# Kernel optimization log

Measured on AMD Instinct MI355X. Metric: run time of the kernel, lower is better.

Reference implementation:

```python
import jax, jax.numpy as jnp
import numpy as np

B, N, C, H, D, K = 8, 2000, 64, 64, 16, 2  # batch, nodes, hidden, hidden_hidden, embed_dim, cheb_k


def setup_inputs() -> dict:
    key = jax.random.key(0)
    ks = jax.random.split(key, 12)
    f = lambda k, s, sc=1.0: jax.random.normal(k, s, dtype=jnp.float32) * sc
    return {
        "z": f(ks[0], (B, N, C)),
        "W_in": f(ks[1], (H, C), 0.1),
        "b_in": f(ks[2], (H,), 0.1),
        "W_out": f(ks[3], (C * C, H), 0.05),
        "b_out": f(ks[4], (C * C,), 0.05),
        "emb": f(ks[5], (N, D), 0.1),
        "wp": f(ks[6], (D, K, H, H), 0.1),
        "bp": f(ks[7], (D, H), 0.1),
        "w1": f(ks[8], (C,)),
        "w2": f(ks[9], (C,)),
        "vs": f(ks[10], (N, N), 0.02),
        "bs": f(ks[11], (N, N), 0.02),
    }


def reference(z, W_in, b_in, W_out, b_out, emb, wp, bp, w1, w2, vs, bs):
    # linear_in + relu: (B,N,C) -> (B,N,H)
    h = jax.nn.relu(jnp.einsum("bnc,hc->bnh", z, W_in) + b_in)

    # data-adaptive graph: softmax over rows of relu(emb @ emb^T)
    A = jax.nn.softmax(jax.nn.relu(emb @ emb.T), axis=1)  # (N,N)
    S = jnp.stack([jnp.eye(N, dtype=z.dtype), A], axis=0)  # (K,N,N), cheb_k=2

    # spatial attention on h (x = h.unsqueeze(1), f_in == H == C)
    e1 = h @ w1  # (B,N)
    e2 = h @ w2  # (B,N)
    prod = e1[:, :, None] * e2[:, None, :]  # (B,N,N) outer product
    E = jax.nn.softmax(
        jnp.einsum("nm,bmp->bnp", vs, jax.nn.sigmoid(prod + bs)), axis=-1
    )  # (B,N,N)

    # batched supports: E.unsqueeze(1) @ S -> (B,K,N,N)
    sup = jnp.einsum("bnm,kmp->bknp", E, S)

    # node-adaptive weights / bias
    weights = jnp.einsum("nd,dkio->nkio", emb, wp)  # (N,K,H,H)
    bias = emb @ bp  # (N,H)

    # graph conv
    x_g = jnp.einsum("bknm,bmc->bnkc", sup, h)  # (B,N,K,H)
    g = jnp.einsum("bnki,nkio->bno", x_g, weights) + bias  # (B,N,H)

    # linear_out + view + tanh, scaled by 0.1
    out = jnp.tanh(jnp.einsum("bnh,oh->bno", g, W_out) + b_out)
    return 0.1 * out.reshape(B, N, C, C)
```

## Files before the change

kernel.cpp:

```cpp
#include <hip/hip_runtime.h>
#include <hip/hip_bf16.h>

#define NN 2000
#define NP 2048
#define BB 8
#define HH 64
#define DD 16

typedef __hip_bfloat16 bf16;
typedef short bf16x8 __attribute__((ext_vector_type(8)));
typedef float f32x4 __attribute__((ext_vector_type(4)));

__device__ __forceinline__ float fast_sigmoid(float x) {
    return 1.0f / (1.0f + __expf(-x));
}
__device__ __forceinline__ float fast_tanh(float x) {
    float e = __expf(2.0f * x);
    return 1.0f - 2.0f / (e + 1.0f);
}

__device__ __forceinline__ void glds16(const void* g, void* l) {
    __builtin_amdgcn_global_load_lds(
        (const __attribute__((address_space(1))) void*)g,
        (__attribute__((address_space(3))) void*)l, 16, 0, 0);
}

__global__ __launch_bounds__(256) void k_h(
        const float* __restrict__ z, const float* __restrict__ W_in,
        const float* __restrict__ b_in, const float* __restrict__ w1,
        const float* __restrict__ w2, float* __restrict__ h,
        float* __restrict__ e1, float* __restrict__ e2) {
    __shared__ float WT[64 * 65];
    __shared__ float zs[4][64];
    int t = threadIdx.x;
    int lane = t & 63, ty = t >> 6;
    int bn0 = blockIdx.x * 4;
    for (int i = t; i < 64 * 64; i += 256) {
        int hh = i >> 6, c = i & 63;
        WT[c * 65 + hh] = W_in[i];
    }
    zs[ty][lane] = z[(size_t)(bn0 + ty) * 64 + lane];
    __syncthreads();
    float acc = b_in[lane];
    #pragma unroll
    for (int c = 0; c < 64; c++) acc += zs[ty][c] * WT[c * 65 + lane];
    float hv = fmaxf(acc, 0.0f);
    h[(size_t)(bn0 + ty) * 64 + lane] = hv;
    float p1 = hv * w1[lane], p2 = hv * w2[lane];
    #pragma unroll
    for (int off = 32; off > 0; off >>= 1) {
        p1 += __shfl_down(p1, off);
        p2 += __shfl_down(p2, off);
    }
    if (lane == 0) { e1[bn0 + ty] = p1; e2[bn0 + ty] = p2; }
}

__global__ __launch_bounds__(256) void k_A(const float* __restrict__ emb,
                                           bf16* __restrict__ A) {
    int i = blockIdx.x, t = threadIdx.x;
    if (i >= NN) {
        for (int j = t; j < NP; j += 256) A[(size_t)i * NP + j] = __float2bfloat16(0.0f);
        return;
    }
    __shared__ float ei[DD];
    __shared__ float rowbuf[NP];
    __shared__ float red[256];
    if (t < DD) ei[t] = emb[i * DD + t];
    __syncthreads();
    float lmax = -1e30f;
    for (int j = t; j < NP; j += 256) {
        float s = 0.0f;
        if (j < NN) {
            #pragma unroll
            for (int d = 0; d < DD; d++) s += ei[d] * emb[j * DD + d];
            s = fmaxf(s, 0.0f);
            lmax = fmaxf(lmax, s);
        }
        rowbuf[j] = s;
    }
    red[t] = lmax; __syncthreads();
    for (int o = 128; o > 0; o >>= 1) { if (t < o) red[t] = fmaxf(red[t], red[t + o]); __syncthreads(); }
    float mx = red[0];
    __syncthreads();
    float lsum = 0.0f;
    for (int j = t; j < NN; j += 256) {
        float e = __expf(rowbuf[j] - mx);
        rowbuf[j] = e; lsum += e;
    }
    red[t] = lsum; __syncthreads();
    for (int o = 128; o > 0; o >>= 1) { if (t < o) red[t] += red[t + o]; __syncthreads(); }
    float inv = 1.0f / red[0];
    for (int j = t; j < NP; j += 256)
        A[(size_t)i * NP + j] = __float2bfloat16(j < NN ? rowbuf[j] * inv : 0.0f);
}

__global__ void k_cvt_vs(const float* __restrict__ vs, bf16* __restrict__ out) {
    int id = blockIdx.x * 256 + threadIdx.x;
    int n = id >> 11, m = id & (NP - 1);
    float v = (n < NN && m < NN) ? vs[n * NN + m] : 0.0f;
    out[id] = __float2bfloat16(v);
}

__global__ void k_cvt_wout(const float* __restrict__ W_out, bf16* __restrict__ out) {
    int id = blockIdx.x * 256 + threadIdx.x;
    out[id] = __float2bfloat16(W_out[id]);
}

__global__ __launch_bounds__(256) void k_hT(const float* __restrict__ h,
                                            bf16* __restrict__ hTcat,
                                            bf16* __restrict__ hsT) {
    __shared__ float tile[64 * 65];
    int nt = blockIdx.x, b = blockIdx.y;
    int tx = threadIdx.x & 63, ty = threadIdx.x >> 6;
    int n0 = nt * 64;
    for (int i = ty * 16; i < ty * 16 + 16; i++) {
        int n = n0 + i;
        tile[i * 65 + tx] = (n < NN) ? h[((size_t)b * NN + n) * 64 + tx] : 0.0f;
    }
    __syncthreads();
    for (int i = ty * 16; i < ty * 16 + 16; i++) {
        bf16 v = __float2bfloat16(tile[tx * 65 + i]);
        hTcat[((size_t)b * 64 + i) * NP + n0 + tx] = v;
        hsT[((size_t)b * 128 + i) * NP + n0 + tx] = v;
    }
}

__global__ __launch_bounds__(256) void k_AhT(const float* __restrict__ Ahcat,
                                             bf16* __restrict__ hsT) {
    __shared__ float tile[64 * 65];
    int pt = blockIdx.x, b = blockIdx.y;
    int tx = threadIdx.x & 63, ty = threadIdx.x >> 6;
    int p0 = pt * 64, q0 = b * 64;
    for (int i = ty * 16; i < ty * 16 + 16; i++)
        tile[i * 65 + tx] = Ahcat[((size_t)p0 + i) * 512 + q0 + tx];
    __syncthreads();
    for (int i = ty * 16; i < ty * 16 + 16; i++)
        hsT[((size_t)b * 128 + 64 + i) * NP + p0 + tx] =
            __float2bfloat16(tile[tx * 65 + i]);
}

__global__ __launch_bounds__(256) void k_Tt(const float* __restrict__ e1,
                                            const float* __restrict__ e2,
                                            const float* __restrict__ bs,
                                            bf16* __restrict__ Tt) {
    __shared__ float tile[64 * 65];
    int b = blockIdx.z;
    e1 += (size_t)b * NN;
    e2 += (size_t)b * NN;
    Tt += (size_t)b * NP * NP;
    int mt = blockIdx.x, pt = blockIdx.y;
    int tx = threadIdx.x & 63, ty = threadIdx.x >> 6;
    int m0 = mt * 64, p0 = pt * 64;
    int p = p0 + tx;
    float e2v = (p < NN) ? e2[p] : 0.0f;
    for (int i = ty * 16; i < ty * 16 + 16; i++) {
        int m = m0 + i;
        float v = 0.0f;
        if (m < NN && p < NN)
            v = fast_sigmoid(e1[m] * e2v + bs[(size_t)m * NN + p]);
        tile[i * 65 + tx] = v;
    }
    __syncthreads();
    for (int i = ty * 16; i < ty * 16 + 16; i++)
        Tt[((size_t)p0 + i) * NP + m0 + tx] = __float2bfloat16(tile[tx * 65 + i]);
}

__global__ __launch_bounds__(256) void k_smax(const float* __restrict__ M,
                                              bf16* __restrict__ E) {
    int n = blockIdx.x, t = threadIdx.x, b = blockIdx.y;
    M += (size_t)b * NP * NP;
    E += (size_t)b * NP * NP;
    short* erow = (short*)(E + (size_t)n * NP);
    int base = t * 8;
    if (n >= NN) {
        bf16x8 zv;
        #pragma unroll
        for (int k = 0; k < 8; k++) zv[k] = 0;
        *(bf16x8*)(erow + base) = zv;
        return;
    }
    __shared__ float red[256];
    const float* row = M + (size_t)n * NP;
    f32x4 v0 = *(const f32x4*)(row + base);
    f32x4 v1 = *(const f32x4*)(row + base + 4);
    float x0 = v0[0], x1 = v0[1], x2 = v0[2], x3 = v0[3];
    float x4 = v1[0], x5 = v1[1], x6 = v1[2], x7 = v1[3];
    float lmax = -1e30f;
    #define MAXK(k, xv) if (base + k < NN) lmax = fmaxf(lmax, xv);
    MAXK(0, x0) MAXK(1, x1) MAXK(2, x2) MAXK(3, x3)
    MAXK(4, x4) MAXK(5, x5) MAXK(6, x6) MAXK(7, x7)
    #undef MAXK
    red[t] = lmax; __syncthreads();
    for (int o = 128; o > 0; o >>= 1) { if (t < o) red[t] = fmaxf(red[t], red[t + o]); __syncthreads(); }
    float mx = red[0];
    __syncthreads();
    float e0, e1v, e2v, e3, e4, e5, e6, e7;
    #define EXPK(k, xv, ev) ev = (base + k < NN) ? __expf(xv - mx) : 0.0f;
    EXPK(0, x0, e0) EXPK(1, x1, e1v) EXPK(2, x2, e2v) EXPK(3, x3, e3)
    EXPK(4, x4, e4) EXPK(5, x5, e5)  EXPK(6, x6, e6)  EXPK(7, x7, e7)
    #undef EXPK
    float lsum = ((e0 + e1v) + (e2v + e3)) + ((e4 + e5) + (e6 + e7));
    red[t] = lsum; __syncthreads();
    for (int o = 128; o > 0; o >>= 1) { if (t < o) red[t] += red[t + o]; __syncthreads(); }
    float inv = 1.0f / red[0];
    bf16x8 ov;
    #define PACK(k, ev) { bf16 bv = __float2bfloat16(ev * inv); ov[k] = *(short*)&bv; }
    PACK(0, e0) PACK(1, e1v) PACK(2, e2v) PACK(3, e3)
    PACK(4, e4) PACK(5, e5)  PACK(6, e6)  PACK(7, e7)
    #undef PACK
    *(bf16x8*)(erow + base) = ov;
}

__global__ __launch_bounds__(512) void k_gemm256(
        const bf16* __restrict__ X, const bf16* __restrict__ Yt,
        float* __restrict__ C, int K, int ldx, int ldy, int ldc,
        long long sX, long long sY, long long sC) {
    __shared__ short As[2 * 256 * 64];
    __shared__ short Bs[2 * 256 * 64];
    int z = blockIdx.z;
    const bf16* Xp = X + (long long)z * sX;
    const bf16* Yp = Yt + (long long)z * sY;
    float* Cp = C + (long long)z * sC;
    int tid = threadIdx.x;
    int m0 = blockIdx.x * 256, n0 = blockIdx.y * 256;
    int wave = tid >> 6, lane = tid & 63;
    int wr = wave >> 2, wc = wave & 3;
    int fr = lane & 15, kq = lane >> 4;

    f32x4 zero = {0.f, 0.f, 0.f, 0.f};
    f32x4 acc[8][4];
    #pragma unroll
    for (int i = 0; i < 8; i++)
        #pragma unroll
        for (int j = 0; j < 4; j++) acc[i][j] = zero;

    int r8 = tid >> 3;
    int sslot = (tid & 7) ^ (r8 & 7);
    const bf16* xsrc = Xp + (long long)(m0 + r8) * ldx + sslot * 8;
    const bf16* ysrc = Yp + (long long)(n0 + r8) * ldy + sslot * 8;

    auto STAGE = [&](int tile) {
        short* Ab = As + (tile & 1) * 16384 + tid * 8;
        short* Bb = Bs + (tile & 1) * 16384 + tid * 8;
        int ko = tile * 64;
        #pragma unroll
        for (int c = 0; c < 4; c++) {
            glds16(xsrc + (long long)(c * 64) * ldx + ko, Ab + c * 4096);
            glds16(ysrc + (long long)(c * 64) * ldy + ko, Bb + c * 4096);
        }
    };

    int NT = K >> 6;
    STAGE(0);
    STAGE(1);
    asm volatile("s_waitcnt vmcnt(8)" ::: "memory");
    __builtin_amdgcn_s_barrier();

    for (int t = 0; t < NT; t++) {
        const short* Ab = As + (t & 1) * 16384 + wr * 8192 + fr * 64;
        const short* Bb = Bs + (t & 1) * 16384 + wc * 4096 + fr * 64;
        #pragma unroll
        for (int ks = 0; ks < 2; ks++) {
            int s = ((ks * 4 + kq) ^ (fr & 7)) * 8;
            bf16x8 a[8], b[4];
            #pragma unroll
            for (int i = 0; i < 8; i++)
                a[i] = *(const bf16x8*)(Ab + i * 1024 + s);
            #pragma unroll
            for (int j = 0; j < 4; j++)
                b[j] = *(const bf16x8*)(Bb + j * 1024 + s);
            __builtin_amdgcn_s_setprio(1);
            #pragma unroll
            for (int i = 0; i < 8; i++)
                #pragma unroll
                for (int j = 0; j < 4; j++)
                    acc[i][j] = __builtin_amdgcn_mfma_f32_16x16x32_bf16(a[i], b[j], acc[i][j], 0, 0, 0);
            __builtin_amdgcn_s_setprio(0);
        }
        __builtin_amdgcn_sched_barrier(0);
        __builtin_amdgcn_s_barrier();
        __builtin_amdgcn_sched_barrier(0);
        if (t + 2 < NT) {
            STAGE(t + 2);
            asm volatile("s_waitcnt vmcnt(8)" ::: "memory");
            __builtin_amdgcn_s_barrier();
        } else if (t + 1 < NT) {
            asm volatile("s_waitcnt vmcnt(0)" ::: "memory");
            __builtin_amdgcn_s_barrier();
        }
    }

    int rq = kq * 4;
    #pragma unroll
    for (int i = 0; i < 8; i++)
        #pragma unroll
        for (int j = 0; j < 4; j++) {
            int col = n0 + wc * 64 + j * 16 + fr;
            long long rowb = m0 + wr * 128 + i * 16 + rq;
            #pragma unroll
            for (int r = 0; r < 4; r++)
                Cp[(rowb + r) * (long long)ldc + col] = acc[i][j][r];
        }
}

template<bool TANH, int KSPLIT>
__global__ __launch_bounds__(256) void k_gemm_bt(
        const bf16* __restrict__ X, const bf16* __restrict__ Yt,
        float* __restrict__ C, const float* __restrict__ bias,
        int K, int ldx, int ldy, int ldc,
        long long sX, long long sY, long long sC, long long sSlice) {
    __shared__ short As[128 * 32];
    __shared__ short Bs[128 * 32];
    int zz = blockIdx.z;
    int ks = 0;
    if (KSPLIT > 1) { ks = zz % KSPLIT; zz /= KSPLIT; }
    const bf16* Xp = X + (long long)zz * sX;
    const bf16* Yp = Yt + (long long)zz * sY;
    float* Cp = C + (long long)zz * sC + (long long)ks * sSlice;
    int tid = threadIdx.x;
    int m0 = blockIdx.x * 128, n0 = blockIdx.y * 128;
    int wave = tid >> 6, lane = tid & 63;
    int wm = (wave >> 1) * 64, wn = (wave & 1) * 64;
    int fr = lane & 15, kq = lane >> 4;

    f32x4 zero = {0.f, 0.f, 0.f, 0.f};
    f32x4 acc[4][4];
    #pragma unroll
    for (int i = 0; i < 4; i++)
        #pragma unroll
        for (int j = 0; j < 4; j++) acc[i][j] = zero;

    int lrow = lane >> 2, lcol = (lane & 3) * 8;
    const bf16* xg0 = Xp + (long long)(m0 + wave * 16 + lrow) * ldx + lcol;
    const bf16* xg1 = xg0 + (long long)64 * ldx;
    const bf16* yg0 = Yp + (long long)(n0 + wave * 16 + lrow) * ldy + lcol;
    const bf16* yg1 = yg0 + (long long)64 * ldy;
    short* lA0 = As + wave * 512;
    short* lA1 = As + (wave + 4) * 512;
    short* lB0 = Bs + wave * 512;
    short* lB1 = Bs + (wave + 4) * 512;

    int kbeg = (KSPLIT > 1) ? ks * (K / KSPLIT) : 0;
    int kend = kbeg + K / KSPLIT;
    for (int k0 = kbeg; k0 < kend; k0 += 32) {
        __syncthreads();
        glds16(xg0 + k0, lA0);
        glds16(xg1 + k0, lA1);
        glds16(yg0 + k0, lB0);
        glds16(yg1 + k0, lB1);
        __syncthreads();
        bf16x8 a[4], b[4];
        #pragma unroll
        for (int i = 0; i < 4; i++)
            a[i] = *(const bf16x8*)(As + (wm + i * 16 + fr) * 32 + kq * 8);
        #pragma unroll
        for (int j = 0; j < 4; j++)
            b[j] = *(const bf16x8*)(Bs + (wn + j * 16 + fr) * 32 + kq * 8);
        #pragma unroll
        for (int i = 0; i < 4; i++)
            #pragma unroll
            for (int j = 0; j < 4; j++)
                acc[i][j] = __builtin_amdgcn_mfma_f32_16x16x32_bf16(a[i], b[j], acc[i][j], 0, 0, 0);
    }
    int rq = kq * 4;
    for (int i = 0; i < 4; i++)
        for (int j = 0; j < 4; j++) {
            int col = n0 + wn + j * 16 + fr;
            float bv = TANH ? bias[col] : 0.0f;
            #pragma unroll
            for (int r = 0; r < 4; r++) {
                int row = m0 + wm + i * 16 + rq + r;
                float v = acc[i][j][r];
                Cp[(long long)row * ldc + col] =
                    TANH ? 0.1f * fast_tanh(v + bv) : v;
            }
        }
}

__global__ __launch_bounds__(256) void k_reduce4(const float* __restrict__ part,
                                                 float* __restrict__ out, int total) {
    int i = (blockIdx.x * 256 + threadIdx.x) * 4;
    f32x4 a = *(const f32x4*)(part + i);
    f32x4 b = *(const f32x4*)(part + (size_t)total + i);
    f32x4 c = *(const f32x4*)(part + (size_t)2 * total + i);
    f32x4 d = *(const f32x4*)(part + (size_t)3 * total + i);
    *(f32x4*)(out + i) = (a + b) + (c + d);
}

__global__ __launch_bounds__(256) void k_g(
        const float* __restrict__ emb, const float* __restrict__ wp,
        const float* __restrict__ bp, const float* __restrict__ xg,
        bf16* __restrict__ gbf) {
    __shared__ float Wn[8192];
    __shared__ float xgs[1024];
    __shared__ float embs[16];
    __shared__ float biass[64];
    int n = blockIdx.x, t = threadIdx.x;
    if (t < 16) embs[t] = emb[n * 16 + t];
    __syncthreads();
    for (int s = 0; s < 32; s++) {
        int e = t + s * 256;
        int j = e >> 6, o = e & 63;
        int kk = j >> 6, ii = j & 63;
        float a = 0.f;
        #pragma unroll
        for (int d = 0; d < 16; d++)
            a += embs[d] * wp[(((size_t)d * 2 + kk) * 64 + ii) * 64 + o];
        Wn[e] = a;
    }
    if (t < 64) {
        float a = 0.f;
        #pragma unroll
        for (int d = 0; d < 16; d++) a += embs[d] * bp[d * 64 + t];
        biass[t] = a;
    }
    for (int s = 0; s < 4; s++) {
        int id = t + s * 256;
        int b = id >> 7, j = id & 127;
        xgs[id] = xg[((size_t)b * NP + n) * 128 + j];
    }
    __syncthreads();
    int o = t & 63, bh = t >> 6;
    for (int half = 0; half < 2; half++) {
        int b = bh + half * 4;
        float a = biass[o];
        for (int j = 0; j < 128; j++) a += xgs[b * 128 + j] * Wn[j * 64 + o];
        gbf[((size_t)b * NN + n) * 64 + o] = __float2bfloat16(a);
    }
}

extern "C" void kernel_launch(void* const* d_in, const int* in_sizes, int n_in,
                              void* d_out, int out_size, void* d_ws, size_t ws_size,
                              hipStream_t stream) {
    const float* z     = (const float*)d_in[0];
    const float* W_in  = (const float*)d_in[1];
    const float* b_in  = (const float*)d_in[2];
    const float* W_out = (const float*)d_in[3];
    const float* b_out = (const float*)d_in[4];
    const float* emb   = (const float*)d_in[5];
    const float* wp    = (const float*)d_in[6];
    const float* bp    = (const float*)d_in[7];
    const float* w1    = (const float*)d_in[8];
    const float* w2    = (const float*)d_in[9];
    const float* vs    = (const float*)d_in[10];
    const float* bs    = (const float*)d_in[11];

    char* p = (char*)d_ws;
    auto alloc = [&](size_t bytes) -> char* {
        char* r = p;
        p += (bytes + 255) & ~(size_t)255;
        return r;
    };
    float* h      = (float*)alloc((size_t)BB * NN * 64 * 4);
    float* e1     = (float*)alloc((size_t)BB * NN * 4);
    float* e2     = (float*)alloc((size_t)BB * NN * 4);
    bf16*  A_bf   = (bf16*) alloc((size_t)NP * NP * 2);
    bf16*  vs_bf  = (bf16*) alloc((size_t)NP * NP * 2);
    bf16*  Tt_all = (bf16*) alloc((size_t)BB * NP * NP * 2);
    float* M_all  = (float*)alloc((size_t)BB * NP * NP * 4);
    bf16*  hTcat  = (bf16*) alloc((size_t)512 * NP * 2);
    float* Ahcat  = (float*)alloc((size_t)NP * 512 * 4);
    float* AhPart = (float*)alloc((size_t)4 * NP * 512 * 4);
    bf16*  hsT    = (bf16*) alloc((size_t)BB * 128 * NP * 2);
    float* xg     = (float*)alloc((size_t)BB * NP * 128 * 4);
    float* xgPart = (float*)alloc((size_t)4 * BB * NP * 128 * 4);
    bf16*  gbf    = (bf16*) alloc((size_t)BB * NN * 64 * 2);
    bf16*  Wo_bf  = (bf16*) alloc((size_t)4096 * 64 * 2);
    bf16* E_all = (bf16*)d_out;

    k_h<<<BB * NN / 4, 256, 0, stream>>>(z, W_in, b_in, w1, w2, h, e1, e2);
    k_A<<<NP, 256, 0, stream>>>(emb, A_bf);
    k_cvt_vs<<<(NP * NP) / 256, 256, 0, stream>>>(vs, vs_bf);
    k_cvt_wout<<<(4096 * 64) / 256, 256, 0, stream>>>(W_out, Wo_bf);
    k_hT<<<dim3(NP / 64, BB), 256, 0, stream>>>(h, hTcat, hsT);

    k_gemm_bt<false, 4><<<dim3(16, 4, 4), 256, 0, stream>>>(
        A_bf, hTcat, AhPart, nullptr, NP, NP, NP, 512,
        0, 0, 0, (long long)NP * 512);
    k_reduce4<<<(NP * 512) / 1024, 256, 0, stream>>>(AhPart, Ahcat, NP * 512);
    k_AhT<<<dim3(NP / 64, BB), 256, 0, stream>>>(Ahcat, hsT);

    k_Tt<<<dim3(NP / 64, NP / 64, BB), 256, 0, stream>>>(e1, e2, bs, Tt_all);
    k_gemm256<<<dim3(8, 8, BB), 512, 0, stream>>>(
        vs_bf, Tt_all, M_all, NP, NP, NP, NP,
        0, (long long)NP * NP, (long long)NP * NP);
    k_smax<<<dim3(NP, BB), 256, 0, stream>>>(M_all, E_all);

    k_gemm_bt<false, 4><<<dim3(16, 1, BB * 4), 256, 0, stream>>>(
        E_all, hsT, xgPart, nullptr, NP, NP, NP, 128,
        (long long)NP * NP, (long long)128 * NP, (long long)NP * 128,
        (long long)BB * NP * 128);
    k_reduce4<<<(BB * NP * 128) / 1024, 256, 0, stream>>>(xgPart, xg, BB * NP * 128);

    k_g<<<NN, 256, 0, stream>>>(emb, wp, bp, xg, gbf);
    k_gemm_bt<true, 1><<<dim3(125, 32, 1), 256, 0, stream>>>(
        gbf, Wo_bf, (float*)d_out, b_out, 64, 64, 64, 4096, 0, 0, 0, 0);
}
```

Before: 700.1 us.

## Fuse softmax exp into attention GEMM epilogue and defer normalization

The attention GEMM epilogue now writes exp(M) as bf16 plus per-tile row sums, removing the fp32 M buffer and the separate softmax kernel. Normalization is deferred: k_g scales xg rows by the inverse summed row totals, since the later matmul is linear in each row of E. It also precomputes node-adaptive weights in a separate k_wn kernel instead of recomputing them inside k_g. The exp is taken without max subtraction, which risks overflow if logits are large, and k_wn writes a 64MB fp32 buffer that k_g reads back.

Measured after the change: 646.8 us. 7.6% less time.

```diff
diff --git a/kernel.cpp b/kernel.cpp
--- a/kernel.cpp
+++ b/kernel.cpp
@@ -104,6 +104,40 @@
 __global__ void k_cvt_wout(const float* __restrict__ W_out, bf16* __restrict__ out) {
     int id = blockIdx.x * 256 + threadIdx.x;
     out[id] = __float2bfloat16(W_out[id]);
+}
+
+__global__ __launch_bounds__(256) void k_wn(const float* __restrict__ emb,
+                                            const float* __restrict__ wp,
+                                            float* __restrict__ Wn_all) {
+    __shared__ float embs[128 * 16];
+    int t = threadIdx.x;
+    int n0 = blockIdx.x * 128;
+    int jo = blockIdx.y * 256 + t;
+    float wv[16];
+    #pragma unroll
+    for (int d = 0; d < 16; d++) wv[d] = wp[(size_t)d * 8192 + jo];
+    for (int s = t; s < 128 * 16; s += 256) {
+        int i = s >> 4, d = s & 15;
+        int n = n0 + i;
+        embs[s] = (n < NN) ? emb[n * 16 + d] : 0.f;
+    }
+    __syncthreads();
+    for (int i = 0; i < 128; i++) {
+        int n = n0 + i;
+        if (n >= NN) break;
+        const f32x4* ev = (const f32x4*)&embs[i * 16];
+        f32x4 e0 = ev[0], e1 = ev[1], e2 = ev[2], e3 = ev[3];
+        float a = 0.f;
+        #pragma unroll
+        for (int q = 0; q < 4; q++) a += e0[q] * wv[q];
+        #pragma unroll
+        for (int q = 0; q < 4; q++) a += e1[q] * wv[4 + q];
+        #pragma unroll
+        for (int q = 0; q < 4; q++) a += e2[q] * wv[8 + q];
+        #pragma unroll
+        for (int q = 0; q < 4; q++) a += e3[q] * wv[12 + q];
+        Wn_all[(size_t)n * 8192 + jo] = a;
+    }
 }
 
 __global__ __launch_bounds__(256) void k_hT(const float* __restrict__ h,
@@ -165,62 +199,18 @@
         Tt[((size_t)p0 + i) * NP + m0 + tx] = __float2bfloat16(tile[tx * 65 + i]);
 }
 
-__global__ __launch_bounds__(256) void k_smax(const float* __restrict__ M,
-                                              bf16* __restrict__ E) {
-    int n = blockIdx.x, t = threadIdx.x, b = blockIdx.y;
-    M += (size_t)b * NP * NP;
-    E += (size_t)b * NP * NP;
-    short* erow = (short*)(E + (size_t)n * NP);
-    int base = t * 8;
-    if (n >= NN) {
-        bf16x8 zv;
-        #pragma unroll
-        for (int k = 0; k < 8; k++) zv[k] = 0;
-        *(bf16x8*)(erow + base) = zv;
-        return;
-    }
-    __shared__ float red[256];
-    const float* row = M + (size_t)n * NP;
-    f32x4 v0 = *(const f32x4*)(row + base);
-    f32x4 v1 = *(const f32x4*)(row + base + 4);
-    float x0 = v0[0], x1 = v0[1], x2 = v0[2], x3 = v0[3];
-    float x4 = v1[0], x5 = v1[1], x6 = v1[2], x7 = v1[3];
-    float lmax = -1e30f;
-    #define MAXK(k, xv) if (base + k < NN) lmax = fmaxf(lmax, xv);
-    MAXK(0, x0) MAXK(1, x1) MAXK(2, x2) MAXK(3, x3)
-    MAXK(4, x4) MAXK(5, x5) MAXK(6, x6) MAXK(7, x7)
-    #undef MAXK
-    red[t] = lmax; __syncthreads();
-    for (int o = 128; o > 0; o >>= 1) { if (t < o) red[t] = fmaxf(red[t], red[t + o]); __syncthreads(); }
-    float mx = red[0];
-    __syncthreads();
-    float e0, e1v, e2v, e3, e4, e5, e6, e7;
-    #define EXPK(k, xv, ev) ev = (base + k < NN) ? __expf(xv - mx) : 0.0f;
-    EXPK(0, x0, e0) EXPK(1, x1, e1v) EXPK(2, x2, e2v) EXPK(3, x3, e3)
-    EXPK(4, x4, e4) EXPK(5, x5, e5)  EXPK(6, x6, e6)  EXPK(7, x7, e7)
-    #undef EXPK
-    float lsum = ((e0 + e1v) + (e2v + e3)) + ((e4 + e5) + (e6 + e7));
-    red[t] = lsum; __syncthreads();
-    for (int o = 128; o > 0; o >>= 1) { if (t < o) red[t] += red[t + o]; __syncthreads(); }
-    float inv = 1.0f / red[0];
-    bf16x8 ov;
-    #define PACK(k, ev) { bf16 bv = __float2bfloat16(ev * inv); ov[k] = *(short*)&bv; }
-    PACK(0, e0) PACK(1, e1v) PACK(2, e2v) PACK(3, e3)
-    PACK(4, e4) PACK(5, e5)  PACK(6, e6)  PACK(7, e7)
-    #undef PACK
-    *(bf16x8*)(erow + base) = ov;
-}
-
-__global__ __launch_bounds__(512) void k_gemm256(
+__global__ __launch_bounds__(512) void k_gemm256p(
         const bf16* __restrict__ X, const bf16* __restrict__ Yt,
-        float* __restrict__ C, int K, int ldx, int ldy, int ldc,
-        long long sX, long long sY, long long sC) {
+        bf16* __restrict__ P, float* __restrict__ rowsumP,
+        int K, int ldx, int ldy,
+        long long sY, long long sP) {
     __shared__ short As[2 * 256 * 64];
     __shared__ short Bs[2 * 256 * 64];
+    __shared__ float rsum2[4][256];
     int z = blockIdx.z;
-    const bf16* Xp = X + (long long)z * sX;
+    const bf16* Xp = X;
     const bf16* Yp = Yt + (long long)z * sY;
-    float* Cp = C + (long long)z * sC;
+    bf16* Pp = P + (long long)z * sP;
     int tid = threadIdx.x;
     int m0 = blockIdx.x * 256, n0 = blockIdx.y * 256;
     int wave = tid >> 6, lane = tid & 63;
@@ -292,15 +282,31 @@
 
     int rq = kq * 4;
     #pragma unroll
-    for (int i = 0; i < 8; i++)
-        #pragma unroll
-        for (int j = 0; j < 4; j++) {
-            int col = n0 + wc * 64 + j * 16 + fr;
-            long long rowb = m0 + wr * 128 + i * 16 + rq;
-            #pragma unroll
-            for (int r = 0; r < 4; r++)
-                Cp[(rowb + r) * (long long)ldc + col] = acc[i][j][r];
+    for (int i = 0; i < 8; i++) {
+        #pragma unroll
+        for (int r = 0; r < 4; r++) {
+            int lrow = wr * 128 + i * 16 + rq + r;
+            long long grow = m0 + lrow;
+            float rs = 0.f;
+            #pragma unroll
+            for (int j = 0; j < 4; j++) {
+                int col = n0 + wc * 64 + j * 16 + fr;
+                float e = (col < NN) ? __expf(acc[i][j][r]) : 0.f;
+                Pp[grow * (long long)NP + col] = __float2bfloat16(e);
+                rs += e;
+            }
+            rs += __shfl_xor(rs, 1);
+            rs += __shfl_xor(rs, 2);
+            rs += __shfl_xor(rs, 4);
+            rs += __shfl_xor(rs, 8);
+            if (fr == 0) rsum2[wc][lrow] = rs;
         }
+    }
+    __syncthreads();
+    if (tid < 256) {
+        float s = rsum2[0][tid] + rsum2[1][tid] + rsum2[2][tid] + rsum2[3][tid];
+        rowsumP[((long long)z * 8 + blockIdx.y) * NP + m0 + tid] = s;
+    }
 }
 
 template<bool TANH, int KSPLIT>
@@ -388,36 +394,39 @@
 }
 
 __global__ __launch_bounds__(256) void k_g(
-        const float* __restrict__ emb, const float* __restrict__ wp,
-        const float* __restrict__ bp, const float* __restrict__ xg,
-        bf16* __restrict__ gbf) {
+        const float* __restrict__ Wn_all, const float* __restrict__ bp,
+        const float* __restrict__ emb, const float* __restrict__ xg,
+        const float* __restrict__ rowsumP, bf16* __restrict__ gbf) {
     __shared__ float Wn[8192];
     __shared__ float xgs[1024];
-    __shared__ float embs[16];
     __shared__ float biass[64];
+    __shared__ float invs[8];
     int n = blockIdx.x, t = threadIdx.x;
-    if (t < 16) embs[t] = emb[n * 16 + t];
-    __syncthreads();
-    for (int s = 0; s < 32; s++) {
-        int e = t + s * 256;
-        int j = e >> 6, o = e & 63;
-        int kk = j >> 6, ii = j & 63;
+    if (t < 8) {
+        float s = 0.f;
+        #pragma unroll
+        for (int y = 0; y < 8; y++)
+            s += rowsumP[((size_t)(t * 8 + y)) * NP + n];
+        invs[t] = 1.0f / s;
+    }
+    if (t >= 64 && t < 128) {
+        int o = t - 64;
         float a = 0.f;
         #pragma unroll
-        for (int d = 0; d < 16; d++)
-            a += embs[d] * wp[(((size_t)d * 2 + kk) * 64 + ii) * 64 + o];
-        Wn[e] = a;
-    }
-    if (t < 64) {
-        float a = 0.f;
-        #pragma unroll
-        for (int d = 0; d < 16; d++) a += embs[d] * bp[d * 64 + t];
-        biass[t] = a;
-    }
+        for (int d = 0; d < 16; d++) a += emb[n * 16 + d] * bp[d * 64 + o];
+        biass[o] = a;
+    }
+    {
+        const f32x4* src = (const f32x4*)(Wn_all + (size_t)n * 8192);
+        f32x4* dst = (f32x4*)Wn;
+        #pragma unroll
+        for (int s = 0; s < 8; s++) dst[s * 256 + t] = src[s * 256 + t];
+    }
+    __syncthreads();
     for (int s = 0; s < 4; s++) {
         int id = t + s * 256;
         int b = id >> 7, j = id & 127;
-        xgs[id] = xg[((size_t)b * NP + n) * 128 + j];
+        xgs[id] = xg[((size_t)b * NP + n) * 128 + j] * invs[b];
     }
     __syncthreads();
     int o = t & 63, bh = t >> 6;
@@ -451,27 +460,29 @@
         p += (bytes + 255) & ~(size_t)255;
         return r;
     };
-    float* h      = (float*)alloc((size_t)BB * NN * 64 * 4);
-    float* e1     = (float*)alloc((size_t)BB * NN * 4);
-    float* e2     = (float*)alloc((size_t)BB * NN * 4);
-    bf16*  A_bf   = (bf16*) alloc((size_t)NP * NP * 2);
-    bf16*  vs_bf  = (bf16*) alloc((size_t)NP * NP * 2);
-    bf16*  Tt_all = (bf16*) alloc((size_t)BB * NP * NP * 2);
-    float* M_all  = (float*)alloc((size_t)BB * NP * NP * 4);
-    bf16*  hTcat  = (bf16*) alloc((size_t)512 * NP * 2);
-    float* Ahcat  = (float*)alloc((size_t)NP * 512 * 4);
-    float* AhPart = (float*)alloc((size_t)4 * NP * 512 * 4);
-    bf16*  hsT    = (bf16*) alloc((size_t)BB * 128 * NP * 2);
-    float* xg     = (float*)alloc((size_t)BB * NP * 128 * 4);
-    float* xgPart = (float*)alloc((size_t)4 * BB * NP * 128 * 4);
-    bf16*  gbf    = (bf16*) alloc((size_t)BB * NN * 64 * 2);
-    bf16*  Wo_bf  = (bf16*) alloc((size_t)4096 * 64 * 2);
-    bf16* E_all = (bf16*)d_out;
+    float* h       = (float*)alloc((size_t)BB * NN * 64 * 4);
+    float* e1      = (float*)alloc((size_t)BB * NN * 4);
+    float* e2      = (float*)alloc((size_t)BB * NN * 4);
+    bf16*  A_bf    = (bf16*) alloc((size_t)NP * NP * 2);
+    bf16*  vs_bf   = (bf16*) alloc((size_t)NP * NP * 2);
+    bf16*  Tt_all  = (bf16*) alloc((size_t)BB * NP * NP * 2);
+    bf16*  P_all   = (bf16*) alloc((size_t)BB * NP * NP * 2);
+    float* rowsumP = (float*)alloc((size_t)BB * 8 * NP * 4);
+    bf16*  hTcat   = (bf16*) alloc((size_t)512 * NP * 2);
+    float* Ahcat   = (float*)alloc((size_t)NP * 512 * 4);
+    float* AhPart  = (float*)alloc((size_t)4 * NP * 512 * 4);
+    bf16*  hsT     = (bf16*) alloc((size_t)BB * 128 * NP * 2);
+    float* xg      = (float*)alloc((size_t)BB * NP * 128 * 4);
+    float* xgPart  = (float*)alloc((size_t)4 * BB * NP * 128 * 4);
+    bf16*  gbf     = (bf16*) alloc((size_t)BB * NN * 64 * 2);
+    bf16*  Wo_bf   = (bf16*) alloc((size_t)4096 * 64 * 2);
+    float* Wn_all  = (float*)alloc((size_t)NN * 8192 * 4);
 
     k_h<<<BB * NN / 4, 256, 0, stream>>>(z, W_in, b_in, w1, w2, h, e1, e2);
     k_A<<<NP, 256, 0, stream>>>(emb, A_bf);
     k_cvt_vs<<<(NP * NP) / 256, 256, 0, stream>>>(vs, vs_bf);
     k_cvt_wout<<<(4096 * 64) / 256, 256, 0, stream>>>(W_out, Wo_bf);
+    k_wn<<<dim3(16, 32), 256, 0, stream>>>(emb, wp, Wn_all);
     k_hT<<<dim3(NP / 64, BB), 256, 0, stream>>>(h, hTcat, hsT);
 
     k_gemm_bt<false, 4><<<dim3(16, 4, 4), 256, 0, stream>>>(
@@ -481,18 +492,17 @@
     k_AhT<<<dim3(NP / 64, BB), 256, 0, stream>>>(Ahcat, hsT);
 
     k_Tt<<<dim3(NP / 64, NP / 64, BB), 256, 0, stream>>>(e1, e2, bs, Tt_all);
-    k_gemm256<<<dim3(8, 8, BB), 512, 0, stream>>>(
-        vs_bf, Tt_all, M_all, NP, NP, NP, NP,
-        0, (long long)NP * NP, (long long)NP * NP);
-    k_smax<<<dim3(NP, BB), 256, 0, stream>>>(M_all, E_all);
+    k_gemm256p<<<dim3(8, 8, BB), 512, 0, stream>>>(
+        vs_bf, Tt_all, P_all, rowsumP, NP, NP, NP,
+        (long long)NP * NP, (long long)NP * NP);
 
     k_gemm_bt<false, 4><<<dim3(16, 1, BB * 4), 256, 0, stream>>>(
-        E_all, hsT, xgPart, nullptr, NP, NP, NP, 128,
+        P_all, hsT, xgPart, nullptr, NP, NP, NP, 128,
         (long long)NP * NP, (long long)128 * NP, (long long)NP * 128,
         (long long)BB * NP * 128);
     k_reduce4<<<(BB * NP * 128) / 1024, 256, 0, stream>>>(xgPart, xg, BB * NP * 128);
 
-    k_g<<<NN, 256, 0, stream>>>(emb, wp, bp, xg, gbf);
+    k_g<<<NN, 256, 0, stream>>>(Wn_all, bp, emb, xg, rowsumP, gbf);
     k_gemm_bt<true, 1><<<dim3(125, 32, 1), 256, 0, stream>>>(
         gbf, Wo_bf, (float*)d_out, b_out, 64, 64, 64, 4096, 0, 0, 0, 0);
 }
```
